# Kernel optimization log

Hardware: AMD Instinct MI355X
Metric: run time of the kernel (lower is better)

## Reference

```python
import jax, jax.numpy as jnp
import numpy as np

N, E = 50000, 800000
IN, HID, OUT = 256, 128, 64


def setup_inputs() -> dict:
    key = jax.random.key(0)
    ks = jax.random.split(key, 8)
    x = jax.random.normal(ks[0], (N, IN), dtype=jnp.float32)
    edge_index = jax.random.randint(ks[1], (2, E), 0, N, dtype=jnp.int64)
    # PyG GCNConv: Linear weight [out, in] (glorot-ish), bias [out] (zeros init; use small randn for a nontrivial baseline)
    W1 = jax.random.normal(ks[2], (HID, IN), dtype=jnp.float32) / np.sqrt(IN)
    b1 = jax.random.normal(ks[3], (HID,), dtype=jnp.float32) * 0.01
    Wmu = jax.random.normal(ks[4], (OUT, HID), dtype=jnp.float32) / np.sqrt(HID)
    bmu = jax.random.normal(ks[5], (OUT,), dtype=jnp.float32) * 0.01
    Wlv = jax.random.normal(ks[6], (OUT, HID), dtype=jnp.float32) / np.sqrt(HID)
    blv = jax.random.normal(ks[7], (OUT,), dtype=jnp.float32) * 0.01
    return {"x": x, "edge_index": edge_index, "W1": W1, "b1": b1,
            "Wmu": Wmu, "bmu": bmu, "Wlv": Wlv, "blv": blv}


def reference(x, edge_index, W1, b1, Wmu, bmu, Wlv, blv):
    n = x.shape[0]
    loop = jnp.arange(n, dtype=edge_index.dtype)
    src = jnp.concatenate([edge_index[0], loop])  # [E+N]
    dst = jnp.concatenate([edge_index[1], loop])
    # symmetric normalization with self-loops: deg computed on destinations
    deg = jax.ops.segment_sum(jnp.ones_like(dst, dtype=x.dtype), dst, num_segments=n)
    dis = jax.lax.rsqrt(deg)  # deg >= 1 due to self-loops
    norm = dis[src] * dis[dst]  # [E+N]

    def gcn(h, W, b):
        hw = h @ W.T                                   # [N, out]
        msg = hw[src] * norm[:, None]                  # [E+N, out] gather + scale
        return jax.ops.segment_sum(msg, dst, num_segments=n) + b

    h = jax.nn.relu(gcn(x, W1, b1))
    # dropout(p=0.5) is identity in eval mode
    return (gcn(h, Wmu, bmu), gcn(h, Wlv, blv))
```

## Files before the change

kernel.cpp:

```cpp
#include <hip/hip_runtime.h>

#define N_NODES 50000
#define N_EDGES 800000
#define DIN 256
#define DHID 128
#define DOUT 64
#define NB_SCAN 49

typedef __attribute__((ext_vector_type(8))) short short8;
typedef __attribute__((ext_vector_type(4))) float f32x4;

static __device__ __forceinline__ short f2bf(float f) {
    union { float f; unsigned u; } v; v.f = f;
    unsigned r = v.u + 0x7FFFu + ((v.u >> 16) & 1u);
    return (short)(r >> 16);
}
static __device__ __forceinline__ float bflo(unsigned p) {
    union { unsigned u; float f; } v; v.u = p << 16; return v.f;
}
static __device__ __forceinline__ float bfhi(unsigned p) {
    union { unsigned u; float f; } v; v.u = p & 0xFFFF0000u; return v.f;
}


__global__ void count_kernel(const int* __restrict__ ei, int* __restrict__ cnt,
                             int* __restrict__ loc) {
    int stride = gridDim.x * blockDim.x;
    for (int e = blockIdx.x * blockDim.x + threadIdx.x; e < N_EDGES; e += stride) {
        loc[e] = atomicAdd(&cnt[ei[N_EDGES + e]], 1);
    }
}

__global__ __launch_bounds__(1024) void bsum_kernel(const int* __restrict__ cnt,
                                                    int* __restrict__ bsum) {
    __shared__ int ws[16];
    int tid = threadIdx.x, i = blockIdx.x * 1024 + tid;
    int v = (i < N_NODES) ? cnt[i] : 0;
    #pragma unroll
    for (int off = 32; off >= 1; off >>= 1) v += __shfl_xor(v, off);
    if ((tid & 63) == 0) ws[tid >> 6] = v;
    __syncthreads();
    if (tid == 0) {
        int s = 0;
        #pragma unroll
        for (int w = 0; w < 16; ++w) s += ws[w];
        bsum[blockIdx.x] = s;
    }
}

__global__ void bscan_kernel(const int* __restrict__ bsum, int* __restrict__ bo,
                             int* __restrict__ rowptr) {
    int l = threadIdx.x;
    int v = (l < NB_SCAN) ? bsum[l] : 0;
    int x = v;
    #pragma unroll
    for (int off = 1; off < 64; off <<= 1) {
        int y = __shfl_up(x, off);
        if (l >= off) x += y;
    }
    if (l < NB_SCAN) bo[l] = x - v;
    if (l == 63) rowptr[N_NODES] = x;
}

__global__ __launch_bounds__(1024) void scan_apply_kernel(const int* __restrict__ cnt,
        const int* __restrict__ bo, int* __restrict__ rowptr,
        float* __restrict__ dis) {
    __shared__ int wsum[16];
    int tid = threadIdx.x, i = blockIdx.x * 1024 + tid;
    int lane = tid & 63, wid = tid >> 6;
    int v = (i < N_NODES) ? cnt[i] : 0;
    int x = v;
    #pragma unroll
    for (int off = 1; off < 64; off <<= 1) {
        int y = __shfl_up(x, off);
        if (lane >= off) x += y;
    }
    if (lane == 63) wsum[wid] = x;
    __syncthreads();
    if (tid == 0) {
        int s = 0;
        #pragma unroll
        for (int w = 0; w < 16; ++w) { int t = wsum[w]; wsum[w] = s; s += t; }
    }
    __syncthreads();
    int excl = bo[blockIdx.x] + wsum[wid] + (x - v);
    if (i < N_NODES) {
        rowptr[i] = excl;
        dis[i] = rsqrtf((float)(v + 1));
    }
}


__global__ void fill_kernel(const int* __restrict__ ei, const int* __restrict__ loc,
                            const int* __restrict__ rowptr, int* __restrict__ col) {
    int stride = gridDim.x * blockDim.x;
    for (int e = blockIdx.x * blockDim.x + threadIdx.x; e < N_EDGES; e += stride) {
        int s = ei[e];
        int d = ei[N_EDGES + e];
        col[rowptr[d] + loc[e]] = s;
    }
}


__global__ void wprep_kernel(const float* __restrict__ W1, const float* __restrict__ Wmu,
                             const float* __restrict__ Wlv, short* __restrict__ W1b,
                             short* __restrict__ Wctb) {
    int tid = blockIdx.x * blockDim.x + threadIdx.x;
    if (tid < DHID * DIN) {
        W1b[tid] = f2bf(W1[tid]);
    } else if (tid < DHID * DIN + 2 * DOUT * DHID) {
        int t = tid - DHID * DIN;
        Wctb[t] = f2bf((t < DOUT * DHID) ? Wmu[t] : Wlv[t - DOUT * DHID]);
    }
}


__global__ __launch_bounds__(256) void gemm1_mfma_kernel(const float* __restrict__ x,
        const short* __restrict__ W1b, const float* __restrict__ dis,
        short* __restrict__ u1b) {
    const int lane = threadIdx.x & 63, w = threadIdx.x >> 6;
    const int l15 = lane & 15, kg = lane >> 4;
    const int nb = blockIdx.x * 64;
    const int r0 = nb + w * 16 + l15;
    const bool valid = r0 < N_NODES;
    const float* xrow = x + (size_t)r0 * DIN;

    f32x4 acc[8] = {};
    #pragma unroll
    for (int ks = 0; ks < 8; ++ks) {
        const int k0 = ks * 32 + kg * 8;
        short8 a;
        if (valid) {
            float4 f0 = *(const float4*)(xrow + k0);
            float4 f1 = *(const float4*)(xrow + k0 + 4);
            a[0] = f2bf(f0.x); a[1] = f2bf(f0.y); a[2] = f2bf(f0.z); a[3] = f2bf(f0.w);
            a[4] = f2bf(f1.x); a[5] = f2bf(f1.y); a[6] = f2bf(f1.z); a[7] = f2bf(f1.w);
        } else {
            a = short8{0, 0, 0, 0, 0, 0, 0, 0};
        }
        #pragma unroll
        for (int c = 0; c < 8; ++c) {
            short8 b = *(const short8*)(W1b + (size_t)(c * 16 + l15) * DIN + k0);
            acc[c] = __builtin_amdgcn_mfma_f32_16x16x32_bf16(a, b, acc[c], 0, 0, 0);
        }
    }

    const int rb = nb + w * 16 + kg * 4;
    float dv[4];
    #pragma unroll
    for (int e = 0; e < 4; ++e) dv[e] = (rb + e < N_NODES) ? dis[rb + e] : 0.f;
    #pragma unroll
    for (int c = 0; c < 8; ++c) {
        #pragma unroll
        for (int e = 0; e < 4; ++e) {
            int r = rb + e;
            if (r < N_NODES)
                u1b[(size_t)r * DHID + c * 16 + l15] = f2bf(acc[c][e] * dv[e]);
        }
    }
}


template <bool LAYER1>
__global__ __launch_bounds__(256) void pull_kernel(const int* __restrict__ rowptr,
        const int* __restrict__ col, const short* __restrict__ uin,
        const float* __restrict__ dis, const float* __restrict__ b1,
        unsigned* __restrict__ uout) {
    const int wid = threadIdx.x >> 6, lane = threadIdx.x & 63;
    const int i = blockIdx.x * 4 + wid;
    if (i >= N_NODES) return;
    const int beg = rowptr[i], end = rowptr[i + 1];
    const unsigned* __restrict__ up = (const unsigned*)uin;
    float ax = 0.f, ay = 0.f;
    for (int base = beg; base < end; base += 64) {
        const int rem = end - base;
        const int m = rem < 64 ? rem : 64;
        int cv = (lane < m) ? col[base + lane] : 0;
        int t = 0;
        for (; t + 8 <= m; t += 8) {
            int c0 = __shfl(cv, t);
            int c1 = __shfl(cv, t + 1);
            int c2 = __shfl(cv, t + 2);
            int c3 = __shfl(cv, t + 3);
            int c4 = __shfl(cv, t + 4);
            int c5 = __shfl(cv, t + 5);
            int c6 = __shfl(cv, t + 6);
            int c7 = __shfl(cv, t + 7);
            unsigned v0 = up[(size_t)c0 * 64 + lane];
            unsigned v1 = up[(size_t)c1 * 64 + lane];
            unsigned v2 = up[(size_t)c2 * 64 + lane];
            unsigned v3 = up[(size_t)c3 * 64 + lane];
            unsigned v4 = up[(size_t)c4 * 64 + lane];
            unsigned v5 = up[(size_t)c5 * 64 + lane];
            unsigned v6 = up[(size_t)c6 * 64 + lane];
            unsigned v7 = up[(size_t)c7 * 64 + lane];
            ax += bflo(v0); ay += bfhi(v0);
            ax += bflo(v1); ay += bfhi(v1);
            ax += bflo(v2); ay += bfhi(v2);
            ax += bflo(v3); ay += bfhi(v3);
            ax += bflo(v4); ay += bfhi(v4);
            ax += bflo(v5); ay += bfhi(v5);
            ax += bflo(v6); ay += bfhi(v6);
            ax += bflo(v7); ay += bfhi(v7);
        }
        for (; t + 4 <= m; t += 4) {
            int c0 = __shfl(cv, t);
            int c1 = __shfl(cv, t + 1);
            int c2 = __shfl(cv, t + 2);
            int c3 = __shfl(cv, t + 3);
            unsigned v0 = up[(size_t)c0 * 64 + lane];
            unsigned v1 = up[(size_t)c1 * 64 + lane];
            unsigned v2 = up[(size_t)c2 * 64 + lane];
            unsigned v3 = up[(size_t)c3 * 64 + lane];
            ax += bflo(v0); ay += bfhi(v0);
            ax += bflo(v1); ay += bfhi(v1);
            ax += bflo(v2); ay += bfhi(v2);
            ax += bflo(v3); ay += bfhi(v3);
        }
        for (; t < m; ++t) {
            int c = __shfl(cv, t);
            unsigned v = up[(size_t)c * 64 + lane];
            ax += bflo(v); ay += bfhi(v);
        }
    }
    const float di = dis[i];
    const unsigned sv = up[(size_t)i * 64 + lane];
    float tx = di * (ax + bflo(sv));
    float ty = di * (ay + bfhi(sv));
    if (LAYER1) {
        float2 b = *(const float2*)(b1 + lane * 2);
        tx = fmaxf(tx + b.x, 0.f) * di;
        ty = fmaxf(ty + b.y, 0.f) * di;
    }
    unsigned o = ((unsigned)(unsigned short)f2bf(tx)) |
                 (((unsigned)(unsigned short)f2bf(ty)) << 16);
    uout[(size_t)i * 64 + lane] = o;
}


__global__ __launch_bounds__(256) void gemm2_mfma_kernel(const short* __restrict__ a2b,
        const short* __restrict__ Wctb, const float* __restrict__ bmu,
        const float* __restrict__ blv, float* __restrict__ out) {
    const int lane = threadIdx.x & 63, w = threadIdx.x >> 6;
    const int l15 = lane & 15, kg = lane >> 4;
    const int nb = blockIdx.x * 64;
    const int r0 = nb + w * 16 + l15;
    const bool valid = r0 < N_NODES;
    const short* arow = a2b + (size_t)r0 * DHID;

    f32x4 acc[8] = {};
    #pragma unroll
    for (int ks = 0; ks < 4; ++ks) {
        const int k0 = ks * 32 + kg * 8;
        short8 a = valid ? *(const short8*)(arow + k0)
                         : short8{0, 0, 0, 0, 0, 0, 0, 0};
        #pragma unroll
        for (int c = 0; c < 8; ++c) {
            short8 b = *(const short8*)(Wctb + (size_t)(c * 16 + l15) * DHID + k0);
            acc[c] = __builtin_amdgcn_mfma_f32_16x16x32_bf16(a, b, acc[c], 0, 0, 0);
        }
    }

    float bias[8];
    #pragma unroll
    for (int c = 0; c < 8; ++c) {
        int j = c * 16 + l15;
        bias[c] = (j < DOUT) ? bmu[j] : blv[j - DOUT];
    }
    const int rb = nb + w * 16 + kg * 4;
    #pragma unroll
    for (int c = 0; c < 8; ++c) {
        const int j = c * 16 + l15;
        float* dst = (j < DOUT) ? (out + j)
                                : (out + (size_t)N_NODES * DOUT + (j - DOUT));
        #pragma unroll
        for (int e = 0; e < 4; ++e) {
            int r = rb + e;
            if (r < N_NODES)
                dst[(size_t)r * DOUT] = acc[c][e] + bias[c];
        }
    }
}


extern "C" void kernel_launch(void* const* d_in, const int* in_sizes, int n_in,
                              void* d_out, int out_size, void* d_ws, size_t ws_size,
                              hipStream_t stream) {
    const float* x   = (const float*)d_in[0];
    const int*   ei  = (const int*)d_in[1];
    const float* W1  = (const float*)d_in[2];
    const float* b1  = (const float*)d_in[3];
    const float* Wmu = (const float*)d_in[4];
    const float* bmu = (const float*)d_in[5];
    const float* Wlv = (const float*)d_in[6];
    const float* blv = (const float*)d_in[7];
    float* out = (float*)d_out;

    char* ws = (char*)d_ws;
    size_t off = 0;
    auto alloc = [&](size_t bytes) -> char* {
        char* p = ws + off;
        off += (bytes + 255) & ~(size_t)255;
        return p;
    };
    int*   cnt    = (int*)  alloc((size_t)N_NODES * 4);
    int*   rowptr = (int*)  alloc((size_t)(N_NODES + 1) * 4);
    float* dis    = (float*)alloc((size_t)N_NODES * 4);
    int*   loc    = (int*)  alloc((size_t)N_EDGES * 4);
    int*   col    = (int*)  alloc((size_t)N_EDGES * 4);
    int*   bsum   = (int*)  alloc((size_t)NB_SCAN * 4);
    int*   bo     = (int*)  alloc((size_t)NB_SCAN * 4);
    short* W1b    = (short*)alloc((size_t)DHID * DIN * 2);
    short* Wctb   = (short*)alloc((size_t)2 * DOUT * DHID * 2);
    short* u1b    = (short*)alloc((size_t)N_NODES * DHID * 2);
    short* u2b    = (short*)alloc((size_t)N_NODES * DHID * 2);
    short* a2b    = (short*)alloc((size_t)N_NODES * DHID * 2);

    hipMemsetAsync(cnt, 0, (size_t)N_NODES * 4, stream);
    wprep_kernel<<<192, 256, 0, stream>>>(W1, Wmu, Wlv, W1b, Wctb);
    count_kernel<<<1024, 256, 0, stream>>>(ei, cnt, loc);
    bsum_kernel<<<NB_SCAN, 1024, 0, stream>>>(cnt, bsum);
    bscan_kernel<<<1, 64, 0, stream>>>(bsum, bo, rowptr);
    scan_apply_kernel<<<NB_SCAN, 1024, 0, stream>>>(cnt, bo, rowptr, dis);
    fill_kernel<<<1024, 256, 0, stream>>>(ei, loc, rowptr, col);
    gemm1_mfma_kernel<<<(N_NODES + 63) / 64, 256, 0, stream>>>(x, W1b, dis, u1b);
    pull_kernel<true><<<N_NODES / 4, 256, 0, stream>>>(rowptr, col, u1b, dis, b1,
                                                       (unsigned*)u2b);
    pull_kernel<false><<<N_NODES / 4, 256, 0, stream>>>(rowptr, col, u2b, dis, nullptr,
                                                        (unsigned*)a2b);
    gemm2_mfma_kernel<<<(N_NODES + 63) / 64, 256, 0, stream>>>(a2b, Wctb, bmu, blv, out);
}
```

Baseline: 274.4 us.

## Pad CSR rows to multiples of eight with zero-row sentinels; hoist gemm1 loads

Each destination row in the CSR is padded up to a multiple of 8 entries, with the padding pointing to an extra all-zero sentinel row appended to the feature buffers. The pull kernel can then drop its 4-wide and scalar tail loops and always gather in groups of 8, which removes divergent remainder handling. Separately, gemm1 now issues all x loads up front before converting to bf16 and running the MFMAs, which should give more memory-level parallelism at the cost of extra registers. Padding adds wasted gathers (up to 7 per node) that read the sentinel row.

```diff
diff --git a/kernel.cpp b/kernel.cpp
--- a/kernel.cpp
+++ b/kernel.cpp
@@ -6,6 +6,7 @@
 #define DHID 128
 #define DOUT 64
 #define NB_SCAN 49
+#define SENT N_NODES
 
 typedef __attribute__((ext_vector_type(8))) short short8;
 typedef __attribute__((ext_vector_type(4))) float f32x4;
@@ -36,6 +37,7 @@
     __shared__ int ws[16];
     int tid = threadIdx.x, i = blockIdx.x * 1024 + tid;
     int v = (i < N_NODES) ? cnt[i] : 0;
+    v = (v + 7) & ~7;
     #pragma unroll
     for (int off = 32; off >= 1; off >>= 1) v += __shfl_xor(v, off);
     if ((tid & 63) == 0) ws[tid >> 6] = v;
@@ -64,12 +66,13 @@
 
 __global__ __launch_bounds__(1024) void scan_apply_kernel(const int* __restrict__ cnt,
         const int* __restrict__ bo, int* __restrict__ rowptr,
-        float* __restrict__ dis) {
+        float* __restrict__ dis, int* __restrict__ col) {
     __shared__ int wsum[16];
     int tid = threadIdx.x, i = blockIdx.x * 1024 + tid;
     int lane = tid & 63, wid = tid >> 6;
     int v = (i < N_NODES) ? cnt[i] : 0;
-    int x = v;
+    int p = (v + 7) & ~7;
+    int x = p;
     #pragma unroll
     for (int off = 1; off < 64; off <<= 1) {
         int y = __shfl_up(x, off);
@@ -83,13 +86,13 @@
         for (int w = 0; w < 16; ++w) { int t = wsum[w]; wsum[w] = s; s += t; }
     }
     __syncthreads();
-    int excl = bo[blockIdx.x] + wsum[wid] + (x - v);
+    int excl = bo[blockIdx.x] + wsum[wid] + (x - p);
     if (i < N_NODES) {
         rowptr[i] = excl;
         dis[i] = rsqrtf((float)(v + 1));
-    }
-}
-
+        for (int q = v; q < p; ++q) col[excl + q] = SENT;
+    }
+}
 
 __global__ void fill_kernel(const int* __restrict__ ei, const int* __restrict__ loc,
                             const int* __restrict__ rowptr, int* __restrict__ col) {
@@ -125,23 +128,35 @@
     const bool valid = r0 < N_NODES;
     const float* xrow = x + (size_t)r0 * DIN;
 
-    f32x4 acc[8] = {};
+    float4 f0[8], f1[8];
     #pragma unroll
     for (int ks = 0; ks < 8; ++ks) {
         const int k0 = ks * 32 + kg * 8;
-        short8 a;
         if (valid) {
-            float4 f0 = *(const float4*)(xrow + k0);
-            float4 f1 = *(const float4*)(xrow + k0 + 4);
-            a[0] = f2bf(f0.x); a[1] = f2bf(f0.y); a[2] = f2bf(f0.z); a[3] = f2bf(f0.w);
-            a[4] = f2bf(f1.x); a[5] = f2bf(f1.y); a[6] = f2bf(f1.z); a[7] = f2bf(f1.w);
+            f0[ks] = *(const float4*)(xrow + k0);
+            f1[ks] = *(const float4*)(xrow + k0 + 4);
         } else {
-            a = short8{0, 0, 0, 0, 0, 0, 0, 0};
-        }
+            f0[ks] = float4{0.f, 0.f, 0.f, 0.f};
+            f1[ks] = float4{0.f, 0.f, 0.f, 0.f};
+        }
+    }
+    short8 a[8];
+    #pragma unroll
+    for (int ks = 0; ks < 8; ++ks) {
+        a[ks][0] = f2bf(f0[ks].x); a[ks][1] = f2bf(f0[ks].y);
+        a[ks][2] = f2bf(f0[ks].z); a[ks][3] = f2bf(f0[ks].w);
+        a[ks][4] = f2bf(f1[ks].x); a[ks][5] = f2bf(f1[ks].y);
+        a[ks][6] = f2bf(f1[ks].z); a[ks][7] = f2bf(f1[ks].w);
+    }
+
+    f32x4 acc[8] = {};
+    #pragma unroll
+    for (int ks = 0; ks < 8; ++ks) {
+        const int k0 = ks * 32 + kg * 8;
         #pragma unroll
         for (int c = 0; c < 8; ++c) {
             short8 b = *(const short8*)(W1b + (size_t)(c * 16 + l15) * DIN + k0);
-            acc[c] = __builtin_amdgcn_mfma_f32_16x16x32_bf16(a, b, acc[c], 0, 0, 0);
+            acc[c] = __builtin_amdgcn_mfma_f32_16x16x32_bf16(a[ks], b, acc[c], 0, 0, 0);
         }
     }
 
@@ -175,9 +190,8 @@
     for (int base = beg; base < end; base += 64) {
         const int rem = end - base;
         const int m = rem < 64 ? rem : 64;
-        int cv = (lane < m) ? col[base + lane] : 0;
-        int t = 0;
-        for (; t + 8 <= m; t += 8) {
+        int cv = (lane < m) ? col[base + lane] : SENT;
+        for (int t = 0; t < m; t += 8) {
             int c0 = __shfl(cv, t);
             int c1 = __shfl(cv, t + 1);
             int c2 = __shfl(cv, t + 2);
@@ -203,25 +217,6 @@
             ax += bflo(v6); ay += bfhi(v6);
             ax += bflo(v7); ay += bfhi(v7);
         }
-        for (; t + 4 <= m; t += 4) {
-            int c0 = __shfl(cv, t);
-            int c1 = __shfl(cv, t + 1);
-            int c2 = __shfl(cv, t + 2);
-            int c3 = __shfl(cv, t + 3);
-            unsigned v0 = up[(size_t)c0 * 64 + lane];
-            unsigned v1 = up[(size_t)c1 * 64 + lane];
-            unsigned v2 = up[(size_t)c2 * 64 + lane];
-            unsigned v3 = up[(size_t)c3 * 64 + lane];
-            ax += bflo(v0); ay += bfhi(v0);
-            ax += bflo(v1); ay += bfhi(v1);
-            ax += bflo(v2); ay += bfhi(v2);
-            ax += bflo(v3); ay += bfhi(v3);
-        }
-        for (; t < m; ++t) {
-            int c = __shfl(cv, t);
-            unsigned v = up[(size_t)c * 64 + lane];
-            ax += bflo(v); ay += bfhi(v);
-        }
     }
     const float di = dis[i];
     const unsigned sv = up[(size_t)i * 64 + lane];
@@ -303,25 +298,28 @@
         off += (bytes + 255) & ~(size_t)255;
         return p;
     };
+    const size_t COL_CAP = (size_t)N_EDGES + 8 * (size_t)N_NODES + 64;
     int*   cnt    = (int*)  alloc((size_t)N_NODES * 4);
     int*   rowptr = (int*)  alloc((size_t)(N_NODES + 1) * 4);
     float* dis    = (float*)alloc((size_t)N_NODES * 4);
     int*   loc    = (int*)  alloc((size_t)N_EDGES * 4);
-    int*   col    = (int*)  alloc((size_t)N_EDGES * 4);
+    int*   col    = (int*)  alloc(COL_CAP * 4);
     int*   bsum   = (int*)  alloc((size_t)NB_SCAN * 4);
     int*   bo     = (int*)  alloc((size_t)NB_SCAN * 4);
     short* W1b    = (short*)alloc((size_t)DHID * DIN * 2);
     short* Wctb   = (short*)alloc((size_t)2 * DOUT * DHID * 2);
-    short* u1b    = (short*)alloc((size_t)N_NODES * DHID * 2);
-    short* u2b    = (short*)alloc((size_t)N_NODES * DHID * 2);
+    short* u1b    = (short*)alloc((size_t)(N_NODES + 1) * DHID * 2);
+    short* u2b    = (short*)alloc((size_t)(N_NODES + 1) * DHID * 2);
     short* a2b    = (short*)alloc((size_t)N_NODES * DHID * 2);
 
     hipMemsetAsync(cnt, 0, (size_t)N_NODES * 4, stream);
+    hipMemsetAsync(u1b + (size_t)N_NODES * DHID, 0, DHID * 2, stream);
+    hipMemsetAsync(u2b + (size_t)N_NODES * DHID, 0, DHID * 2, stream);
     wprep_kernel<<<192, 256, 0, stream>>>(W1, Wmu, Wlv, W1b, Wctb);
     count_kernel<<<1024, 256, 0, stream>>>(ei, cnt, loc);
     bsum_kernel<<<NB_SCAN, 1024, 0, stream>>>(cnt, bsum);
     bscan_kernel<<<1, 64, 0, stream>>>(bsum, bo, rowptr);
-    scan_apply_kernel<<<NB_SCAN, 1024, 0, stream>>>(cnt, bo, rowptr, dis);
+    scan_apply_kernel<<<NB_SCAN, 1024, 0, stream>>>(cnt, bo, rowptr, dis, col);
     fill_kernel<<<1024, 256, 0, stream>>>(ei, loc, rowptr, col);
     gemm1_mfma_kernel<<<(N_NODES + 63) / 64, 256, 0, stream>>>(x, W1b, dis, u1b);
     pull_kernel<true><<<N_NODES / 4, 256, 0, stream>>>(rowptr, col, u1b, dis, b1,
```

Result: slower. 281.9 us (+2.7%).
